# Performance work log

Measured on AMD Instinct MI355X. Metric: run time of the kernel, lower is better.

The kernel has to match this reference:

```python
import jax, jax.numpy as jnp
import numpy as np

B, L, D_MODEL = 2, 2048, 768
H, F = 12, 16            # num_heads, feature_dim
DH = D_MODEL // H        # head_dim = 64


def setup_inputs() -> dict:
    key = jax.random.key(0)
    ks = jax.random.split(key, 5)
    scale = lambda fan_in: 1.0 / np.sqrt(fan_in)
    return {
        "hidden_states": jax.random.normal(ks[0], (B, L, D_MODEL), jnp.float32),
        "Wq": jax.random.normal(ks[1], (D_MODEL, H * F), jnp.float32) * scale(D_MODEL),
        "Wk": jax.random.normal(ks[2], (D_MODEL, H * F), jnp.float32) * scale(D_MODEL),
        "Wv": jax.random.normal(ks[3], (D_MODEL, H * DH), jnp.float32) * scale(D_MODEL),
        "Wo": jax.random.normal(ks[4], (H * DH, D_MODEL), jnp.float32) * scale(H * DH),
    }


def reference(hidden_states, Wq, Wk, Wv, Wo):
    b, l, d = hidden_states.shape
    dt = hidden_states.dtype
    # projections -> (b, h, l, feat)
    q = (hidden_states @ Wq).reshape(b, l, H, F).transpose(0, 2, 1, 3)
    k = (hidden_states @ Wk).reshape(b, l, H, F).transpose(0, 2, 1, 3)
    v = (hidden_states @ Wv).reshape(b, l, H, DH).transpose(0, 2, 1, 3)

    n = jnp.arange(1, l + 1, dtype=dt)[:, None]          # (l, 1)
    mean_keys = jnp.cumsum(k, axis=2) / n                # running mean over seq
    center_keys = k - mean_keys
    mean_values = jnp.cumsum(v, axis=2) / n
    center_values = v - mean_values

    qK = jnp.einsum('bhqi,bhpi->bhqp', q, center_keys)   # (b,h,l,l)
    causal = jnp.tril(jnp.ones((l, l), dtype=bool))
    qK = jnp.where(causal, qK, jnp.zeros((), dt))

    inv_2d = 1.0 / (2.0 * DH)
    # cumsum over query dim, then sum over key dim (faithful to original)
    qK_squared = jnp.sum(jnp.cumsum(qK * qK * inv_2d, axis=2), axis=3)  # (b,h,l)
    denominator = n[:, 0] + qK_squared                   # (b,h,l) via broadcast

    qKV = jnp.einsum('bhqp,bhpi->bhqi', qK, center_values) / jnp.sqrt(jnp.asarray(DH, dt))
    y = mean_values + qKV / denominator[..., None]       # (b,h,l,dh)
    y = y.transpose(0, 2, 1, 3).reshape(b, l, H * DH)
    return y @ Wo
```

## Files before the change

### kernel.cpp

```cpp
#include <hip/hip_runtime.h>
#include <hip/hip_bf16.h>
#include <stdint.h>

constexpr int B_ = 2, L_ = 2048, DM = 768, NH_ = 12, F_ = 16, DH_ = 64;
constexpr int CH = 32, NCH = L_ / CH;

typedef __bf16 bf16x8 __attribute__((ext_vector_type(8)));
typedef __bf16 bf16x4 __attribute__((ext_vector_type(4)));
typedef float f32x4 __attribute__((ext_vector_type(4)));
typedef float f32x16 __attribute__((ext_vector_type(16)));
typedef unsigned u32x2 __attribute__((ext_vector_type(2)));

#define GLOAD16(g, l)                                                        \
  __builtin_amdgcn_global_load_lds(                                          \
      (const __attribute__((address_space(1))) void*)(g),                    \
      (__attribute__((address_space(3))) void*)(l), 16, 0, 0)

__device__ __forceinline__ unsigned cvt_pk_bf16(float lo, float hi) {
  unsigned r;
  asm("v_cvt_pk_bf16_f32 %0, %1, %2" : "=v"(r) : "v"(lo), "v"(hi));
  return r;
}

union pa_u { unsigned u[4]; bf16x8 v; };

__device__ __forceinline__ void pack_p(const f32x16& s, pa_u& pa0, pa_u& pa1) {
  unsigned w0 = cvt_pk_bf16(s[0], s[1]),   w1 = cvt_pk_bf16(s[2], s[3]);
  unsigned w2 = cvt_pk_bf16(s[4], s[5]),   w3 = cvt_pk_bf16(s[6], s[7]);
  unsigned w4 = cvt_pk_bf16(s[8], s[9]),   w5 = cvt_pk_bf16(s[10], s[11]);
  unsigned w6 = cvt_pk_bf16(s[12], s[13]), w7 = cvt_pk_bf16(s[14], s[15]);
  u32x2 r0 = __builtin_amdgcn_permlane32_swap(w0, w2, false, false);
  u32x2 r1 = __builtin_amdgcn_permlane32_swap(w1, w3, false, false);
  u32x2 r2 = __builtin_amdgcn_permlane32_swap(w4, w6, false, false);
  u32x2 r3 = __builtin_amdgcn_permlane32_swap(w5, w7, false, false);
  pa0.u[0] = r0[0]; pa0.u[1] = r1[0]; pa0.u[2] = r0[1]; pa0.u[3] = r1[1];
  pa1.u[0] = r2[0]; pa1.u[1] = r3[0]; pa1.u[2] = r2[1]; pa1.u[3] = r3[1];
}

__global__ __launch_bounds__(256)
void prep_kernel(const float* __restrict__ hs, const float* __restrict__ Wq,
                 const float* __restrict__ Wk, const float* __restrict__ Wv,
                 const float* __restrict__ Wo, __bf16* __restrict__ hsb,
                 __bf16* __restrict__ WqkvT, __bf16* __restrict__ WoT) {
  int bx = blockIdx.x;
  if (bx < 1440) {
    const float* src; __bf16* dst; int C, kt, nt;
    int id = bx;
    if (id < 144)      { src = Wq; dst = WqkvT;             C = 192; kt = id / 6;  nt = id % 6;  }
    else if (id < 288) { id -= 144; src = Wk; dst = WqkvT + (size_t)192 * 768; C = 192; kt = id / 6;  nt = id % 6;  }
    else if (id < 864) { id -= 288; src = Wv; dst = WqkvT + (size_t)384 * 768; C = 768; kt = id / 24; nt = id % 24; }
    else               { id -= 864; src = Wo; dst = WoT;    C = 768; kt = id / 24; nt = id % 24; }
    __shared__ float ld[32][33];
    int tid = threadIdx.x;
    int r = tid >> 3, cg = tid & 7;
    int k0 = kt * 32, n0 = nt * 32;
    float4 v = *(const float4*)(src + (size_t)(k0 + r) * C + n0 + cg * 4);
    ld[r][cg * 4 + 0] = v.x;
    ld[r][cg * 4 + 1] = v.y;
    ld[r][cg * 4 + 2] = v.z;
    ld[r][cg * 4 + 3] = v.w;
    __syncthreads();
    int nl = tid >> 3, kg = tid & 7;
    bf16x4 o;
#pragma unroll
    for (int j = 0; j < 4; j++) o[j] = (__bf16)ld[kg * 4 + j][nl];
    *(bf16x4*)(dst + (size_t)(n0 + nl) * 768 + k0 + kg * 4) = o;
  } else {
    int base = (bx - 1440) * 2048 + threadIdx.x * 8;
    float4 a = *(const float4*)(hs + base);
    float4 b4 = *(const float4*)(hs + base + 4);
    bf16x8 o;
    o[0] = (__bf16)a.x;  o[1] = (__bf16)a.y;  o[2] = (__bf16)a.z;  o[3] = (__bf16)a.w;
    o[4] = (__bf16)b4.x; o[5] = (__bf16)b4.y; o[6] = (__bf16)b4.z; o[7] = (__bf16)b4.w;
    *(bf16x8*)(hsb + base) = o;
  }
}

__global__ __launch_bounds__(256)
void gemm_proj(const __bf16* __restrict__ A, const __bf16* __restrict__ Bt,
               int K, __bf16* __restrict__ Qh, __bf16* __restrict__ Kh,
               __bf16* __restrict__ Vh, float* __restrict__ csum) {
  __shared__ __align__(16) __bf16 Al[3][128 * 32];
  __shared__ __align__(16) __bf16 Bl[3][64 * 32];
  __shared__ float csl[4][64];
  int tid = threadIdx.x;
  int m0 = blockIdx.y * 128, n0 = blockIdx.x * 64;
  int w = tid >> 6, l = tid & 63, lr = l & 15, lg = l >> 4;
  int rowb = w * 32;
  f32x4 acc[2][4] = {};
  const __bf16* Ab = A + (size_t)m0 * K;
  const __bf16* Bb = Bt + (size_t)n0 * K;
  int nt = K / 32;
  auto stage = [&](int buf, int k0) {
#pragma unroll
    for (int i = 0; i < 2; i++) {
      int idx = i * 256 + tid;
      GLOAD16(Ab + (size_t)(idx >> 2) * K + k0 + (idx & 3) * 8, &Al[buf][idx * 8]);
    }
    GLOAD16(Bb + (size_t)(tid >> 2) * K + k0 + (tid & 3) * 8, &Bl[buf][tid * 8]);
  };
  stage(0, 0);
  stage(1, 32);
  for (int t = 0; t < nt; t++) {
    if (t + 1 < nt) {
      asm volatile("s_waitcnt vmcnt(3)" ::: "memory");
    } else {
      asm volatile("s_waitcnt vmcnt(0)" ::: "memory");
    }
    __syncthreads();
    if (t + 2 < nt) stage((t + 2) % 3, (t + 2) * 32);
    int cur = t % 3;
    bf16x8 af[2], bfr[4];
#pragma unroll
    for (int mi = 0; mi < 2; mi++)
      af[mi] = *(const bf16x8*)&Al[cur][(rowb + mi * 16 + lr) * 32 + lg * 8];
#pragma unroll
    for (int ni = 0; ni < 4; ni++)
      bfr[ni] = *(const bf16x8*)&Bl[cur][(ni * 16 + lr) * 32 + lg * 8];
#pragma unroll
    for (int mi = 0; mi < 2; mi++)
#pragma unroll
      for (int ni = 0; ni < 4; ni++)
        acc[mi][ni] = __builtin_amdgcn_mfma_f32_16x16x32_bf16(
            af[mi], bfr[ni], acc[mi][ni], 0, 0, 0);
  }
#pragma unroll
  for (int mi = 0; mi < 2; mi++)
#pragma unroll
    for (int ni = 0; ni < 4; ni++) {
      int n = n0 + ni * 16 + lr;
#pragma unroll
      for (int r = 0; r < 4; r++) {
        int m = m0 + rowb + mi * 16 + lg * 4 + r;
        float v = acc[mi][ni][r];
        int b = m >> 11, ll = m & 2047;
        if (n < 192)
          Qh[((size_t)(b * NH_ + (n >> 4)) * L_ + ll) * F_ + (n & 15)] = (__bf16)v;
        else if (n < 384)
          Kh[((size_t)(b * NH_ + ((n - 192) >> 4)) * L_ + ll) * F_ + ((n - 192) & 15)] = (__bf16)v;
        else
          Vh[((size_t)(b * NH_ + ((n - 384) >> 6)) * L_ + ll) * DH_ + ((n - 384) & 63)] = (__bf16)v;
      }
    }
#pragma unroll
  for (int ni = 0; ni < 4; ni++) {
    float cs = 0.f;
#pragma unroll
    for (int mi = 0; mi < 2; mi++)
#pragma unroll
      for (int r = 0; r < 4; r++) cs += (float)(__bf16)acc[mi][ni][r];
    cs += __shfl_xor(cs, 16, 64);
    cs += __shfl_xor(cs, 32, 64);
    if (lg == 0) csl[w][ni * 16 + lr] = cs;
  }
  __syncthreads();
  {
    int chs = tid >> 6, colg = tid & 63;
    int n = n0 + colg;
    if (n >= 192) {
      int b = m0 >> 11;
      int ch32 = ((m0 & 2047) >> 5) + chs;
      float v = csl[chs][colg];
      int h, c;
      if (n < 384) { h = (n - 192) >> 4; c = (n - 192) & 15; }
      else         { h = (n - 384) >> 6; c = 16 + ((n - 384) & 63); }
      csum[((size_t)(b * NH_ + h) * NCH + ch32) * 80 + c] = v;
    }
  }
}

__global__ __launch_bounds__(256)
void gemm_out(const __bf16* __restrict__ A, const __bf16* __restrict__ Bt,
              int M, int N, int K, float* __restrict__ C) {
  __shared__ __align__(16) __bf16 Al[3][128 * 32];
  __shared__ __align__(16) __bf16 Bl[3][64 * 32];
  int tid = threadIdx.x;
  int m0 = blockIdx.y * 128, n0 = blockIdx.x * 64;
  int w = tid >> 6, l = tid & 63, lr = l & 15, lg = l >> 4;
  int rowb = w * 32;
  f32x4 acc[2][4] = {};
  const __bf16* Ab = A + (size_t)m0 * K;
  const __bf16* Bb = Bt + (size_t)n0 * K;
  int nt = K / 32;
  auto stage = [&](int buf, int k0) {
#pragma unroll
    for (int i = 0; i < 2; i++) {
      int idx = i * 256 + tid;
      GLOAD16(Ab + (size_t)(idx >> 2) * K + k0 + (idx & 3) * 8, &Al[buf][idx * 8]);
    }
    GLOAD16(Bb + (size_t)(tid >> 2) * K + k0 + (tid & 3) * 8, &Bl[buf][tid * 8]);
  };
  stage(0, 0);
  stage(1, 32);
  for (int t = 0; t < nt; t++) {
    if (t + 1 < nt) {
      asm volatile("s_waitcnt vmcnt(3)" ::: "memory");
    } else {
      asm volatile("s_waitcnt vmcnt(0)" ::: "memory");
    }
    __syncthreads();
    if (t + 2 < nt) stage((t + 2) % 3, (t + 2) * 32);
    int cur = t % 3;
    bf16x8 af[2], bfr[4];
#pragma unroll
    for (int mi = 0; mi < 2; mi++)
      af[mi] = *(const bf16x8*)&Al[cur][(rowb + mi * 16 + lr) * 32 + lg * 8];
#pragma unroll
    for (int ni = 0; ni < 4; ni++)
      bfr[ni] = *(const bf16x8*)&Bl[cur][(ni * 16 + lr) * 32 + lg * 8];
#pragma unroll
    for (int mi = 0; mi < 2; mi++)
#pragma unroll
      for (int ni = 0; ni < 4; ni++)
        acc[mi][ni] = __builtin_amdgcn_mfma_f32_16x16x32_bf16(
            af[mi], bfr[ni], acc[mi][ni], 0, 0, 0);
  }
#pragma unroll
  for (int mi = 0; mi < 2; mi++)
#pragma unroll
    for (int ni = 0; ni < 4; ni++) {
      int n = n0 + ni * 16 + lr;
#pragma unroll
      for (int r = 0; r < 4; r++) {
        int m = m0 + rowb + mi * 16 + lg * 4 + r;
        C[(size_t)m * N + n] = acc[mi][ni][r];
      }
    }
}

__global__ __launch_bounds__(128)
void scan_apply(const __bf16* __restrict__ Kh, const __bf16* __restrict__ Vh,
                const float* __restrict__ csum,
                __bf16* __restrict__ CKh, __bf16* __restrict__ CVf,
                __bf16* __restrict__ Yb) {
  int bh = blockIdx.y, ch = blockIdx.x;
  int b = bh / NH_, h = bh % NH_;
  int c = threadIdx.x;
  if (c >= 80) return;
  float run = 0.f;
  for (int j = 0; j < ch; j++) run += csum[((size_t)bh * NCH + j) * 80 + c];
  if (c < 16) {
    const __bf16* src = Kh + ((size_t)bh * L_ + ch * CH) * F_ + c;
    __bf16* ckp = CKh + ((size_t)bh * L_ + ch * CH) * F_ + c;
    for (int r = 0; r < CH; r++) {
      float val = (float)src[(size_t)r * F_];
      run += val;
      float mean = run * __builtin_amdgcn_rcpf((float)(ch * CH + r + 1));
      ckp[(size_t)r * F_] = (__bf16)(val - mean);
    }
  } else {
    int d = c - 16;
    const __bf16* src = Vh + ((size_t)bh * L_ + ch * CH) * DH_ + d;
    __bf16* cvbase = CVf + (size_t)bh * 128 * 1024;
    __bf16* yp = Yb + ((size_t)(b * L_ + ch * CH)) * DM + h * DH_ + d;
    for (int r = 0; r < CH; r++) {
      float val = (float)src[(size_t)r * DH_];
      run += val;
      int p = ch * CH + r;
      float mean = run * __builtin_amdgcn_rcpf((float)(p + 1));
      cvbase[(size_t)(p >> 4) * 1024 + d * 16 + (p & 15)] = (__bf16)(val - mean);
      yp[(size_t)r * DM] = (__bf16)mean;
    }
  }
}

__global__ __launch_bounds__(256)
void attn_mfma(const __bf16* __restrict__ Qh, const __bf16* __restrict__ CKh,
               const __bf16* __restrict__ CVf, __bf16* __restrict__ qkv,
               float* __restrict__ rs2) {
  __shared__ float slab[4][32][65];
  __shared__ float s2slab[4][32];
  int bh = blockIdx.y;
  int pairi = blockIdx.x;
  int tid = threadIdx.x;
  int w = tid >> 6, l = tid & 63;
  int lp = l & 31, hi = l >> 5;
  const __bf16* ckb = CKh + (size_t)bh * L_ * F_;
  const __bf16* cvb = CVf + (size_t)bh * 128 * 1024;

#pragma unroll
  for (int half = 0; half < 2; half++) {
    int ti = half ? (63 - pairi) : pairi;
    int q0 = ti * 32;
    bf16x8 qb = *(const bf16x8*)(Qh + ((size_t)bh * L_ + q0 + lp) * F_ + hi * 8);
    f32x16 pv0 = {}, pv1 = {};
    float s2 = 0.f;

    int pfirst = (w <= ti) ? w : 0;
    bf16x8 ka = *(const bf16x8*)(ckb + (size_t)(pfirst * 32 + lp) * F_ + hi * 8);
    const __bf16* cvp = cvb + (size_t)(2 * pfirst) * 1024 + lp * 16 + hi * 8;
    bf16x8 bv0 = *(const bf16x8*)(cvp);
    bf16x8 bv1 = *(const bf16x8*)(cvp + 512);
    bf16x8 bv2 = *(const bf16x8*)(cvp + 1024);
    bf16x8 bv3 = *(const bf16x8*)(cvp + 1536);

    for (int pt = w; pt <= ti; pt += 4) {
      int ptn = (pt + 4 <= ti) ? pt + 4 : pt;
      bf16x8 ka_n = *(const bf16x8*)(ckb + (size_t)(ptn * 32 + lp) * F_ + hi * 8);
      const __bf16* cvpn = cvb + (size_t)(2 * ptn) * 1024 + lp * 16 + hi * 8;
      bf16x8 bn0 = *(const bf16x8*)(cvpn);
      bf16x8 bn1 = *(const bf16x8*)(cvpn + 512);
      bf16x8 bn2 = *(const bf16x8*)(cvpn + 1024);
      bf16x8 bn3 = *(const bf16x8*)(cvpn + 1536);

      f32x16 s = {};
      s = __builtin_amdgcn_mfma_f32_32x32x16_bf16(ka, qb, s, 0, 0, 0);
      if (pt == ti) {
#pragma unroll
        for (int reg = 0; reg < 16; reg++) {
          int pidx = (reg & 3) + 8 * (reg >> 2) + 4 * hi;
          if (pidx > lp) s[reg] = 0.f;
        }
      }
#pragma unroll
      for (int reg = 0; reg < 16; reg++) s2 = fmaf(s[reg], s[reg], s2);
      pa_u pa0, pa1;
      pack_p(s, pa0, pa1);
      __builtin_amdgcn_s_setprio(1);
      pv0 = __builtin_amdgcn_mfma_f32_32x32x16_bf16(pa0.v, bv0, pv0, 0, 0, 0);
      pv1 = __builtin_amdgcn_mfma_f32_32x32x16_bf16(pa0.v, bv1, pv1, 0, 0, 0);
      pv0 = __builtin_amdgcn_mfma_f32_32x32x16_bf16(pa1.v, bv2, pv0, 0, 0, 0);
      pv1 = __builtin_amdgcn_mfma_f32_32x32x16_bf16(pa1.v, bv3, pv1, 0, 0, 0);
      __builtin_amdgcn_s_setprio(0);
      ka = ka_n; bv0 = bn0; bv1 = bn1; bv2 = bn2; bv3 = bn3;
    }

    s2 += __shfl_xor(s2, 32, 64);
    if (hi == 0) s2slab[w][lp] = s2;
#pragma unroll
    for (int reg = 0; reg < 16; reg++) {
      int ql = (reg & 3) + 8 * (reg >> 2) + 4 * hi;
      slab[w][ql][lp] = pv0[reg];
      slab[w][ql][32 + lp] = pv1[reg];
    }
    __syncthreads();
    if (tid < 32) {
      float v = s2slab[0][tid] + s2slab[1][tid] + s2slab[2][tid] + s2slab[3][tid];
      rs2[(size_t)bh * L_ + q0 + tid] = v * (1.0f / 128.0f);
    }
    {
      int q = tid >> 3, seg = tid & 7;
      bf16x8 o;
#pragma unroll
      for (int j = 0; j < 8; j++) {
        int d = seg * 8 + j;
        float acc = slab[0][q][d] + slab[1][q][d] + slab[2][q][d] + slab[3][q][d];
        o[j] = (__bf16)(acc * 0.125f);
      }
      *(bf16x8*)(qkv + ((size_t)bh * L_ + q0 + q) * DH_ + seg * 8) = o;
    }
    if (half == 0) __syncthreads();
  }
}

__global__ __launch_bounds__(256)
void combine_kernel(const __bf16* __restrict__ qkv, const float* __restrict__ rs2,
                    __bf16* __restrict__ Yb) {
  int bh = blockIdx.y, lt = blockIdx.x;
  int b = bh / NH_, h = bh % NH_;
  int t = threadIdx.x;
  int l0 = lt * 256;
  __shared__ float part[256];
  __shared__ float dinv[256];
  const float* rs = rs2 + (size_t)bh * L_;
  float vals[8];
  float run = 0.f;
#pragma unroll
  for (int i = 0; i < 8; i++) { run += rs[t * 8 + i]; vals[i] = run; }
  part[t] = run;
  __syncthreads();
  for (int o = 1; o < 256; o <<= 1) {
    float add = (t >= o) ? part[t - o] : 0.f;
    __syncthreads();
    part[t] += add;
    __syncthreads();
  }
  float base = (t > 0) ? part[t - 1] : 0.f;
#pragma unroll
  for (int i = 0; i < 8; i++) {
    int ll = t * 8 + i;
    if (ll >= l0 && ll < l0 + 256)
      dinv[ll - l0] = 1.0f / ((float)(ll + 1) + base + vals[i]);
  }
  __syncthreads();
#pragma unroll
  for (int it = 0; it < 8; it++) {
    int v = it * 256 + t;
    int ll = v >> 3, d8 = v & 7;
    bf16x8 q8 = *(const bf16x8*)(qkv + ((size_t)bh * L_ + l0 + ll) * DH_ + d8 * 8);
    __bf16* yp = Yb + ((size_t)(b * L_ + l0 + ll)) * DM + h * DH_ + d8 * 8;
    bf16x8 y8 = *(const bf16x8*)yp;
    float iv = dinv[ll];
#pragma unroll
    for (int j = 0; j < 8; j++)
      y8[j] = (__bf16)((float)y8[j] + (float)q8[j] * iv);
    *(bf16x8*)yp = y8;
  }
}

extern "C" void kernel_launch(void* const* d_in, const int* in_sizes, int n_in,
                              void* d_out, int out_size, void* d_ws, size_t ws_size,
                              hipStream_t stream) {
  const float* hs = (const float*)d_in[0];
  const float* Wq = (const float*)d_in[1];
  const float* Wk = (const float*)d_in[2];
  const float* Wv = (const float*)d_in[3];
  const float* Wo = (const float*)d_in[4];
  float* out = (float*)d_out;
  char* w = (char*)d_ws;

  __bf16* hsb   = (__bf16*)(w);
  __bf16* WqkvT = (__bf16*)(w + 6291456);
  __bf16* WoT   = (__bf16*)(w + 8060928);
  __bf16* Kh    = (__bf16*)(w + 9240576);
  __bf16* Vh    = (__bf16*)(w + 10813440);
  __bf16* qkvb  = (__bf16*)(w + 28114944);
  __bf16* Qh    = (__bf16*)(w + 34406400);
  __bf16* CKh   = (__bf16*)(w + 35979264);
  __bf16* CVfg  = (__bf16*)(w + 37552128);
  __bf16* Yb    = (__bf16*)(w + 43843584);
  float*  rs2   = (float*)(w + 50135040);
  float*  csum  = (float*)(w + 50331648);

  prep_kernel<<<2976, 256, 0, stream>>>(hs, Wq, Wk, Wv, Wo, hsb, WqkvT, WoT);
  dim3 g1(1152 / 64, (B_ * L_) / 128);
  gemm_proj<<<g1, 256, 0, stream>>>(hsb, WqkvT, DM, Qh, Kh, Vh, csum);
  dim3 gs(NCH, B_ * NH_);
  scan_apply<<<gs, 128, 0, stream>>>(Kh, Vh, csum, CKh, CVfg, Yb);
  dim3 g3(32, 24);
  attn_mfma<<<g3, 256, 0, stream>>>(Qh, CKh, CVfg, qkvb, rs2);
  dim3 g5(8, 24);
  combine_kernel<<<g5, 256, 0, stream>>>(qkvb, rs2, Yb);
  dim3 g6(DM / 64, (B_ * L_) / 128);
  gemm_out<<<g6, 256, 0, stream>>>(Yb, WoT, B_ * L_, DM, DM, out);
}
```

Baseline: 97.00 us.

## Remap workgroups across XCDs and switch GEMMs to double-buffered LDS pipeline

```diff
diff --git a/kernel.cpp b/kernel.cpp
--- a/kernel.cpp
+++ b/kernel.cpp
@@ -20,6 +20,11 @@
   unsigned r;
   asm("v_cvt_pk_bf16_f32 %0, %1, %2" : "=v"(r) : "v"(lo), "v"(hi));
   return r;
+}
+
+__device__ __forceinline__ int xcd_swizzle(int flat, int nwg) {
+  int cpx = nwg >> 3;
+  return (flat & 7) * cpx + (flat >> 3);
 }
 
 union pa_u { unsigned u[4]; bf16x8 v; };
@@ -80,11 +85,13 @@
 void gemm_proj(const __bf16* __restrict__ A, const __bf16* __restrict__ Bt,
                int K, __bf16* __restrict__ Qh, __bf16* __restrict__ Kh,
                __bf16* __restrict__ Vh, float* __restrict__ csum) {
-  __shared__ __align__(16) __bf16 Al[3][128 * 32];
-  __shared__ __align__(16) __bf16 Bl[3][64 * 32];
+  __shared__ __align__(16) __bf16 Al[2][128 * 32];
+  __shared__ __align__(16) __bf16 Bl[2][64 * 32];
   __shared__ float csl[4][64];
   int tid = threadIdx.x;
-  int m0 = blockIdx.y * 128, n0 = blockIdx.x * 64;
+  int flat = blockIdx.x + gridDim.x * blockIdx.y;
+  int swz = xcd_swizzle(flat, gridDim.x * gridDim.y);
+  int m0 = (swz / gridDim.x) * 128, n0 = (swz % gridDim.x) * 64;
   int w = tid >> 6, l = tid & 63, lr = l & 15, lg = l >> 4;
   int rowb = w * 32;
   f32x4 acc[2][4] = {};
@@ -100,16 +107,11 @@
     GLOAD16(Bb + (size_t)(tid >> 2) * K + k0 + (tid & 3) * 8, &Bl[buf][tid * 8]);
   };
   stage(0, 0);
-  stage(1, 32);
+  asm volatile("s_waitcnt vmcnt(0)" ::: "memory");
+  __syncthreads();
+  int cur = 0;
   for (int t = 0; t < nt; t++) {
-    if (t + 1 < nt) {
-      asm volatile("s_waitcnt vmcnt(3)" ::: "memory");
-    } else {
-      asm volatile("s_waitcnt vmcnt(0)" ::: "memory");
-    }
-    __syncthreads();
-    if (t + 2 < nt) stage((t + 2) % 3, (t + 2) * 32);
-    int cur = t % 3;
+    if (t + 1 < nt) stage(cur ^ 1, (t + 1) * 32);
     bf16x8 af[2], bfr[4];
 #pragma unroll
     for (int mi = 0; mi < 2; mi++)
@@ -123,6 +125,9 @@
       for (int ni = 0; ni < 4; ni++)
         acc[mi][ni] = __builtin_amdgcn_mfma_f32_16x16x32_bf16(
             af[mi], bfr[ni], acc[mi][ni], 0, 0, 0);
+    asm volatile("s_waitcnt vmcnt(0)" ::: "memory");
+    __syncthreads();
+    cur ^= 1;
   }
 #pragma unroll
   for (int mi = 0; mi < 2; mi++)
@@ -172,10 +177,12 @@
 __global__ __launch_bounds__(256)
 void gemm_out(const __bf16* __restrict__ A, const __bf16* __restrict__ Bt,
               int M, int N, int K, float* __restrict__ C) {
-  __shared__ __align__(16) __bf16 Al[3][128 * 32];
-  __shared__ __align__(16) __bf16 Bl[3][64 * 32];
+  __shared__ __align__(16) __bf16 Al[2][128 * 32];
+  __shared__ __align__(16) __bf16 Bl[2][64 * 32];
   int tid = threadIdx.x;
-  int m0 = blockIdx.y * 128, n0 = blockIdx.x * 64;
+  int flat = blockIdx.x + gridDim.x * blockIdx.y;
+  int swz = xcd_swizzle(flat, gridDim.x * gridDim.y);
+  int m0 = (swz / gridDim.x) * 128, n0 = (swz % gridDim.x) * 64;
   int w = tid >> 6, l = tid & 63, lr = l & 15, lg = l >> 4;
   int rowb = w * 32;
   f32x4 acc[2][4] = {};
@@ -191,16 +198,11 @@
     GLOAD16(Bb + (size_t)(tid >> 2) * K + k0 + (tid & 3) * 8, &Bl[buf][tid * 8]);
   };
   stage(0, 0);
-  stage(1, 32);
+  asm volatile("s_waitcnt vmcnt(0)" ::: "memory");
+  __syncthreads();
+  int cur = 0;
   for (int t = 0; t < nt; t++) {
-    if (t + 1 < nt) {
-      asm volatile("s_waitcnt vmcnt(3)" ::: "memory");
-    } else {
-      asm volatile("s_waitcnt vmcnt(0)" ::: "memory");
-    }
-    __syncthreads();
-    if (t + 2 < nt) stage((t + 2) % 3, (t + 2) * 32);
-    int cur = t % 3;
+    if (t + 1 < nt) stage(cur ^ 1, (t + 1) * 32);
     bf16x8 af[2], bfr[4];
 #pragma unroll
     for (int mi = 0; mi < 2; mi++)
@@ -214,6 +216,9 @@
       for (int ni = 0; ni < 4; ni++)
         acc[mi][ni] = __builtin_amdgcn_mfma_f32_16x16x32_bf16(
             af[mi], bfr[ni], acc[mi][ni], 0, 0, 0);
+    asm volatile("s_waitcnt vmcnt(0)" ::: "memory");
+    __syncthreads();
+    cur ^= 1;
   }
 #pragma unroll
   for (int mi = 0; mi < 2; mi++)
@@ -270,8 +275,10 @@
                float* __restrict__ rs2) {
   __shared__ float slab[4][32][65];
   __shared__ float s2slab[4][32];
-  int bh = blockIdx.y;
-  int pairi = blockIdx.x;
+  int flat = blockIdx.x + 32 * blockIdx.y;
+  int swz = xcd_swizzle(flat, 32 * 24);
+  int pairi = swz & 31;
+  int bh = swz >> 5;
   int tid = threadIdx.x;
   int w = tid >> 6, l = tid & 63;
   int lp = l & 31, hi = l >> 5;
```

New measurement: 91.12 us. 1.06x faster.
